# Optimization experiments

Measured on AMD Instinct MI355X. Metric: run time of the kernel, lower is better.

## Reference

```python
import jax, jax.numpy as jnp
import numpy as np

B, T, D, C, L, H = 8192, 128, 1, 1, 1, 64


def _mlp(x, w1, b1, w2, b2):
    # Linear -> Softplus -> Linear
    return jax.nn.softplus(x @ w1 + b1) @ w2 + b2


def setup_inputs() -> dict:
    key = jax.random.key(0)
    ks = jax.random.split(key, 32)
    s = 0.1

    def w(k, shape):
        return jax.random.normal(k, shape, jnp.float32) * s

    p = {}
    p["xs"] = jax.random.normal(ks[0], (T, B, D), jnp.float32)
    p["ts"] = jnp.arange(T, dtype=jnp.float32)
    p["noise_std"] = jnp.float32(5.0)
    p["eps0"] = jax.random.normal(ks[1], (B, L), jnp.float32)
    p["dW_std"] = jax.random.normal(ks[2], (T - 1, B, L), jnp.float32)
    # encoder: data -> hidden -> context
    p["ew1"] = w(ks[3], (D, H)); p["eb1"] = w(ks[4], (H,))
    p["ew2"] = w(ks[5], (H, C)); p["eb2"] = w(ks[6], (C,))
    # qz0_net: context -> 2*latent
    p["qw"] = w(ks[7], (C, 2 * L)); p["qb"] = w(ks[8], (2 * L,))
    # f_net: latent+context -> hidden -> latent
    p["fw1"] = w(ks[9], (L + C, H)); p["fb1"] = w(ks[10], (H,))
    p["fw2"] = w(ks[11], (H, L)); p["fb2"] = w(ks[12], (L,))
    # h_net: latent -> hidden -> latent
    p["hw1"] = w(ks[13], (L, H)); p["hb1"] = w(ks[14], (H,))
    p["hw2"] = w(ks[15], (H, L)); p["hb2"] = w(ks[16], (L,))
    # g_nets: L independent 1 -> hidden -> 1 -> sigmoid nets, stacked on leading L axis
    p["gw1"] = w(ks[17], (L, H)); p["gb1"] = w(ks[18], (L, H))
    p["gw2"] = w(ks[19], (L, H)); p["gb2"] = w(ks[20], (L,))
    # projector: latent -> hidden -> data
    p["pw1"] = w(ks[21], (L, H)); p["pb1"] = w(ks[22], (H,))
    p["pw2"] = w(ks[23], (H, D)); p["pb2"] = w(ks[24], (D,))
    p["pz0_mean"] = jnp.zeros((1, L), jnp.float32)
    p["pz0_logstd"] = jnp.zeros((1, L), jnp.float32)
    return p


def reference(xs, ts, noise_std, eps0, dW_std,
              ew1, eb1, ew2, eb2, qw, qb,
              fw1, fb1, fw2, fb2, hw1, hb1, hw2, hb2,
              gw1, gb1, gw2, gb2, pw1, pb1, pw2, pb2,
              pz0_mean, pz0_logstd):
    Tn = ts.shape[0]
    # ctx = flip(encoder(flip(xs)))  (encoder is pointwise in time)
    ctx = jnp.flip(_mlp(jnp.flip(xs, axis=0), ew1, eb1, ew2, eb2), axis=0)  # [T,B,C]
    qz = ctx[0] @ qw + qb
    qm, qls = jnp.split(qz, 2, axis=1)  # [B,L] each
    z0 = qm + jnp.exp(qls) * eps0

    def g_fn(z):  # per-coordinate diagonal diffusion nets
        hid = jax.nn.softplus(z[:, :, None] * gw1[None] + gb1[None])  # [B,L,H]
        return jax.nn.sigmoid(jnp.einsum('blh,lh->bl', hid, gw2) + gb2)

    def step(z, inp):
        k, dwk = inp
        t = ts[k]
        dt = ts[k + 1] - ts[k]
        idx = jnp.minimum(jnp.searchsorted(ts, t, side='right'), Tn - 1)
        c = jnp.take(ctx, idx, axis=0)  # [B,C]
        fv = _mlp(jnp.concatenate([z, c], axis=1), fw1, fb1, fw2, fb2)
        hv = _mlp(z, hw1, hb1, hw2, hb2)
        gv = g_fn(z)
        u = (fv - hv) / gv
        lr = 0.5 * jnp.sum(u * u, axis=1) * dt  # logqp path increment [B]
        z_next = z + fv * dt + gv * dwk * jnp.sqrt(dt)  # Euler-Maruyama
        return z_next, (z_next, lr)

    _, (ztail, log_ratio) = jax.lax.scan(step, z0, (jnp.arange(Tn - 1), dW_std))
    zs = jnp.concatenate([z0[None], ztail], axis=0)  # [T,B,L]
    _xs = _mlp(zs, pw1, pb1, pw2, pb2)  # [T,B,D]
    lp = -0.5 * ((xs - _xs) / noise_std) ** 2 - jnp.log(noise_std) - 0.5 * jnp.log(2 * jnp.pi)
    log_pxs = lp.sum(axis=(0, 2)).mean()
    kl = (pz0_logstd - qls) + (jnp.exp(2 * qls) + (qm - pz0_mean) ** 2) / (2 * jnp.exp(2 * pz0_logstd)) - 0.5
    logqp0 = kl.sum(axis=1).mean()
    logqp_path = log_ratio.sum(axis=0).mean()
    return (log_pxs, logqp0 + logqp_path)
```

## Files before the change

kernel.cpp:

```cpp
#include <hip/hip_runtime.h>
#include <math.h>


#define B_SZ 8192
#define T_SZ 128
#define NBLK 256

#define NT1 1025
#define NT2 1025
#define NEE 1024
#define NENT (NT1 + NT2 + NEE)

#define ENT_F 10
#define ZT_FLOATS (ENT_F * (NT1 + NT2))
#define T2_BASEF (ENT_F * NT1)
#define ET2G_OFF ZT_FLOATS
#define TABG_FLOATS (ZT_FLOATS + 2048)

#define NXI 1024
#define XSF 64.0f
#define XOF 512.0f

#if __has_builtin(__builtin_amdgcn_rcpf)
#define RCPF(x) __builtin_amdgcn_rcpf(x)
#else
#define RCPF(x) (1.0f / (x))
#endif
#if __has_builtin(__builtin_amdgcn_sqrtf)
#define SQRTF(x) __builtin_amdgcn_sqrtf(x)
#else
#define SQRTF(x) sqrtf(x)
#endif

__device__ __forceinline__ float sp_precise(float a) {
  return fmaxf(a, 0.0f) + log1pf(expf(-fabsf(a)));
}
__device__ __forceinline__ float wsum64(float v) {
  #pragma unroll
  for (int m = 1; m <= 32; m <<= 1) v += __shfl_xor(v, m);
  return v;
}
__device__ __forceinline__ float swz4(float v) {
  return __int_as_float(__builtin_amdgcn_ds_swizzle(__float_as_int(v), 0x101F));
}
template <int CTRL>
__device__ __forceinline__ float dpp_mov(float v) {
  return __int_as_float(
      __builtin_amdgcn_update_dpp(0, __float_as_int(v), CTRL, 0xF, 0xF, true));
}

__global__ __launch_bounds__(256) void build_tabs(
    const float* __restrict__ ew1, const float* __restrict__ eb1,
    const float* __restrict__ ew2, const float* __restrict__ eb2,
    const float* __restrict__ fw1, const float* __restrict__ fb1,
    const float* __restrict__ fw2, const float* __restrict__ fb2,
    const float* __restrict__ hw1, const float* __restrict__ hb1,
    const float* __restrict__ hw2, const float* __restrict__ hb2,
    const float* __restrict__ gw1, const float* __restrict__ gb1,
    const float* __restrict__ gw2, const float* __restrict__ gb2,
    const float* __restrict__ pw1, const float* __restrict__ pb1,
    const float* __restrict__ pw2, const float* __restrict__ pb2,
    float* __restrict__ tabs, int* __restrict__ ctr)
{
  const int gtid = blockIdx.x * 256 + threadIdx.x;
  if (gtid == 0) *ctr = 0;
  const int ent  = gtid >> 6;
  const int lane = threadIdx.x & 63;
  if (ent >= NENT) return;

  if (ent < NT1 + NT2) {
    const bool t1 = ent < NT1;
    const int  i  = t1 ? ent : (ent - NT1);
    const float z = t1 ? (-128.0f + (float)i * 0.25f)
                       : (-8192.0f + (float)i * 16.0f);
    const int basef = (t1 ? 0 : T2_BASEF) + ENT_F * i;

    const float az = fmaf(z, fw1[lane], fb1[lane]);
    const float wc = fw1[64 + lane], w2 = fw2[lane];
    float s0 = sp_precise(fmaf(-3.0f, wc, az)) * w2;
    float s1 = sp_precise(fmaf(-1.0f, wc, az)) * w2;
    float s2 = sp_precise(fmaf( 1.0f, wc, az)) * w2;
    float s3 = sp_precise(fmaf( 3.0f, wc, az)) * w2;
    float sh = sp_precise(fmaf(z, hw1[lane], hb1[lane])) * hw2[lane];
    float sg = sp_precise(fmaf(z, gw1[lane], gb1[lane])) * gw2[lane];
    float sp = sp_precise(fmaf(z, pw1[lane], pb1[lane])) * pw2[lane];
    s0 = wsum64(s0); s1 = wsum64(s1); s2 = wsum64(s2); s3 = wsum64(s3);
    sh = wsum64(sh); sg = wsum64(sg); sp = wsum64(sp);
    if (lane == 0) {
      const float fb = fb2[0];
      tabs[basef + 0] = s0 + fb;
      tabs[basef + 1] = s1 + fb;
      tabs[basef + 2] = s2 + fb;
      tabs[basef + 3] = s3 + fb;
      tabs[basef + 4] = sh + hb2[0];
      tabs[basef + 5] = 1.0f / (1.0f + expf(-(sg + gb2[0])));
      tabs[basef + 6] = sp + pb2[0];
      tabs[basef + 7] = 0.0f;
      tabs[basef + 8] = 0.0f;
      tabs[basef + 9] = 0.0f;
    }
  } else {
    const int i = ent - (NT1 + NT2);
    const float x0 = -8.0f + (float)i * (1.0f / 64.0f);
    const float x1 = x0 + (1.0f / 64.0f);
    const float w = ew1[lane], bb = eb1[lane], w2 = ew2[lane];
    float s0 = sp_precise(fmaf(x0, w, bb)) * w2;
    float s1 = sp_precise(fmaf(x1, w, bb)) * w2;
    s0 = wsum64(s0); s1 = wsum64(s1);
    if (lane == 0) {
      const float eb = eb2[0];
      ((float2*)(tabs + ET2G_OFF))[i] = make_float2(s0 + eb, s1 + eb);
    }
  }
}

__global__ __launch_bounds__(256) void ctx_pre(
    const float* __restrict__ xs, const float* __restrict__ tabs,
    float* __restrict__ ctx)
{
  const int i = blockIdx.x * 256 + threadIdx.x;
  const float2* et2 = (const float2*)(tabs + ET2G_OFF);
  const float s = fmaf(xs[i], XSF, XOF);
  const float sc = fminf(fmaxf(s, 0.0f), (float)(NXI - 1));
  const int ii = (int)sc;
  const float fr = s - (float)ii;
  const float2 e = et2[ii];
  ctx[i] = fmaf(fr, e.y - e.x, e.x);
}

__global__ __launch_bounds__(256) void sde_scan(
    const float* __restrict__ xs, const float* __restrict__ ts,
    const float* __restrict__ noise_std, const float* __restrict__ eps0,
    const float* __restrict__ dW, const float* __restrict__ ctx,
    const float* __restrict__ qw,  const float* __restrict__ qb,
    const float* __restrict__ fw1, const float* __restrict__ fb1,
    const float* __restrict__ fw2, const float* __restrict__ fb2,
    const float* __restrict__ hw1, const float* __restrict__ hb1,
    const float* __restrict__ hw2, const float* __restrict__ hb2,
    const float* __restrict__ gw1, const float* __restrict__ gb1,
    const float* __restrict__ gw2, const float* __restrict__ gb2,
    const float* __restrict__ pw1, const float* __restrict__ pb1,
    const float* __restrict__ pw2, const float* __restrict__ pb2,
    const float* __restrict__ pz0_mean, const float* __restrict__ pz0_logstd,
    const float* __restrict__ tabsrc,
    int* __restrict__ ctr, float* __restrict__ partA, float* __restrict__ partB,
    float* __restrict__ out)
{
  __shared__ __align__(16) float tab[ZT_FLOATS];
  __shared__ float la[256], lb[256];
  __shared__ int lastflag;

  const int tid = threadIdx.x;
  const int li  = tid & 7;
  const int b   = blockIdx.x * 32 + (tid >> 3);

  {
    const float4* s4 = (const float4*)tabsrc;
    float4* d4 = (float4*)tab;
    for (int i = tid; i < ZT_FLOATS / 4; i += 256) d4[i] = s4[i];
  }
  __syncthreads();

  const float fb2s = fb2[0], hb2s = hb2[0], gb2s = gb2[0], pb2s = pb2[0];
  const float qw0 = qw[0], qw1 = qw[1], qb0 = qb[0], qb1 = qb[1];
  const float ns = noise_std[0];
  const float inv_ns = 1.0f / ns;
  const float nh_i2 = -0.5f * inv_ns * inv_ns;
  const float pm = pz0_mean[0], pls = pz0_logstd[0];

  auto hgp_exact = [&](float z_, float& hv_, float& gv_, float& pv_) {
    float sh = 0.f, sg = 0.f, sp = 0.f;
    for (int j = 0; j < 64; ++j) {
      sh = fmaf(sp_precise(fmaf(z_, hw1[j], hb1[j])), hw2[j], sh);
      sg = fmaf(sp_precise(fmaf(z_, gw1[j], gb1[j])), gw2[j], sg);
      sp = fmaf(sp_precise(fmaf(z_, pw1[j], pb1[j])), pw2[j], sp);
    }
    hv_ = sh + hb2s;
    gv_ = 1.0f / (1.0f + expf(-(sg + gb2s)));
    pv_ = sp + pb2s;
  };
  auto f_exact = [&](float z_, float c_) {
    float s = 0.f;
    for (int j = 0; j < 64; ++j)
      s = fmaf(sp_precise(fmaf(z_, fw1[j], fmaf(c_, fw1[64 + j], fb1[j]))), fw2[j], s);
    return s + fb2s;
  };
  auto zidx = [&](float z_, int& basef_, float& frac_, bool& inr_) {
    const float s1 = fmaf(z_, 4.0f, 512.0f);
    const float s2v = fmaf(z_, 0.0625f, 512.0f);
    const bool t1 = (s1 >= 0.0f) && (s1 <= 1024.0f);
    const bool t2 = (s2v >= 0.0f) && (s2v <= 1024.0f);
    inr_ = t1 || t2;
    const float sf = t1 ? s1 : fminf(fmaxf(s2v, 0.0f), 1024.0f);
    const int fi = min((int)sf, 1023);
    basef_ = (t1 ? 0 : T2_BASEF) + ENT_F * fi;
    frac_ = sf - (float)fi;
  };

  const float c0v = ctx[b];
  const float qm  = fmaf(c0v, qw0, qb0);
  const float qls = fmaf(c0v, qw1, qb1);
  float z = fmaf(__expf(qls), eps0[b], qm);
  const float dqm = qm - pm;
  const float kl = (pls - qls)
                 + (__expf(2.0f * qls) + dqm * dqm) * (0.5f * __expf(-2.0f * pls))
                 - 0.5f;

  float xbuf0 = xs[0 * B_SZ + b], cbuf0 = ctx[0 * B_SZ + b], wbuf0 = dW[0 * B_SZ + b];
  float xbuf1 = xs[1 * B_SZ + b], cbuf1 = ctx[1 * B_SZ + b], wbuf1 = dW[1 * B_SZ + b];
  float xbuf2 = xs[2 * B_SZ + b], cbuf2 = ctx[2 * B_SZ + b], wbuf2 = dW[2 * B_SZ + b];
  float xbuf3 = xs[3 * B_SZ + b], cbuf3 = ctx[3 * B_SZ + b], wbuf3 = dW[3 * B_SZ + b];

  bool zin; int zb; float zfr;
  zidx(z, zb, zfr, zin);

  float lrs = 0.0f, lps = 0.0f;
  const int part = li & 3;
  const int loff = ((li >> 2) * ENT_F) + 2 * part;

#define STEP(K, J) { \
    const int kc = min((K) + 1, T_SZ - 1); \
    const float dt = ts[kc] - ts[(K)]; \
    const float sq = SQRTF(dt); \
    const float cc = cbuf##J; \
    const float c2 = cc * cc; \
    const float p1c = c2 - 1.0f, p3c = c2 - 9.0f; \
    const float L0 = p1c * (cc - 3.0f) * (-1.0f / 48.0f); \
    const float L1 = p3c * (cc - 1.0f) * ( 1.0f / 16.0f); \
    const float L2 = p3c * (cc + 1.0f) * (-1.0f / 16.0f); \
    const float L3 = p1c * (cc + 3.0f) * ( 1.0f / 48.0f); \
    const bool cin = fabsf(cc) <= 3.0f; \
    const float2 va = *(const float2*)(tab + zb + loff); \
    const float wz = (li < 4) ? (1.0f - zfr) : zfr; \
    const float Asel = (part == 0) ? L0 : ((part == 1) ? L2 : 1.0f); \
    const float Bsel = (part == 0) ? L1 : ((part == 1) ? L3 : 0.0f); \
    const float r0 = wz * fmaf(Asel, va.x, Bsel * va.y); \
    const float r1 = wz * va.y; \
    const float u0 = r0 + swz4(r0); \
    const float u1 = r1 + swz4(r1); \
    const float fv01 = u0 + dpp_mov<0xB1>(u0); \
    const float X = (part < 2) ? fv01 : u0; \
    const float xX = dpp_mov<0x4E>(X); \
    const float xY = dpp_mov<0x4E>(u1); \
    float FV = (part < 2) ? fv01 : xX; \
    float HV = (part == 0) ? xX : u0; \
    float GV = (part == 0) ? xY : u1; \
    float PV = (part == 1) ? xX : u0; \
    if (!(zin && cin)) FV = f_exact(z, cc); \
    if (!zin) { float he, ge, pe; hgp_exact(z, he, ge, pe); HV = he; GV = ge; PV = pe; } \
    const float gvs = fmaxf(GV, 1e-6f); \
    const float uu = (FV - HV) * RCPF(gvs); \
    lrs = fmaf((0.5f * dt) * uu, uu, lrs); \
    const float zn = fmaf(gvs * wbuf##J, sq, fmaf(FV, dt, z)); \
    const float znb = dpp_mov<0xB1>(zn); \
    z = (li & 1) ? znb : zn; \
    const float d_ = xbuf##J - PV; \
    lps = fmaf(nh_i2 * d_, d_, lps); \
     \
    const int kk_ = (K) + 4; \
    const int ixc_ = min(kk_, T_SZ - 1) * B_SZ + b; \
    const float xb_n = xs[ixc_]; \
    const float cb_n = ctx[ixc_]; \
    const float wb_n = (kk_ < T_SZ - 1) ? dW[kk_ * B_SZ + b] : 0.0f; \
    zidx(z, zb, zfr, zin); \
    xbuf##J = xb_n; cbuf##J = cb_n; wbuf##J = wb_n; \
  }

  for (int k = 0; k < T_SZ; k += 4) {
    STEP(k, 0); STEP(k + 1, 1); STEP(k + 2, 2); STEP(k + 3, 3);
  }
#undef STEP

  la[tid] = (li == 1) ? lps : 0.0f;
  lb[tid] = (li == 0) ? (kl + lrs) : 0.0f;
  __syncthreads();
  for (int s = 128; s > 0; s >>= 1) {
    if (tid < s) { la[tid] += la[tid + s]; lb[tid] += lb[tid + s]; }
    __syncthreads();
  }
  if (tid == 0) {
    partA[blockIdx.x] = la[0]; partB[blockIdx.x] = lb[0];
    __threadfence();
    lastflag = (atomicAdd(ctr, 1) == NBLK - 1) ? 1 : 0;
  }
  __syncthreads();
  if (lastflag) {
    __threadfence();
    la[tid] = partA[tid]; lb[tid] = partB[tid];
    __syncthreads();
    for (int s = 128; s > 0; s >>= 1) {
      if (tid < s) { la[tid] += la[tid + s]; lb[tid] += lb[tid + s]; }
      __syncthreads();
    }
    if (tid == 0) {
      out[0] = la[0] / (float)B_SZ
             + (float)T_SZ * (-__logf(ns) - 0.9189385332046727f);
      out[1] = lb[0] / (float)B_SZ;
    }
  }
}

extern "C" void kernel_launch(void* const* d_in, const int* in_sizes, int n_in,
                              void* d_out, int out_size, void* d_ws, size_t ws_size,
                              hipStream_t stream) {
  const float* xs        = (const float*)d_in[0];
  const float* ts        = (const float*)d_in[1];
  const float* noise_std = (const float*)d_in[2];
  const float* eps0      = (const float*)d_in[3];
  const float* dW        = (const float*)d_in[4];
  const float* ew1 = (const float*)d_in[5];
  const float* eb1 = (const float*)d_in[6];
  const float* ew2 = (const float*)d_in[7];
  const float* eb2 = (const float*)d_in[8];
  const float* qw  = (const float*)d_in[9];
  const float* qb  = (const float*)d_in[10];
  const float* fw1 = (const float*)d_in[11];
  const float* fb1 = (const float*)d_in[12];
  const float* fw2 = (const float*)d_in[13];
  const float* fb2 = (const float*)d_in[14];
  const float* hw1 = (const float*)d_in[15];
  const float* hb1 = (const float*)d_in[16];
  const float* hw2 = (const float*)d_in[17];
  const float* hb2 = (const float*)d_in[18];
  const float* gw1 = (const float*)d_in[19];
  const float* gb1 = (const float*)d_in[20];
  const float* gw2 = (const float*)d_in[21];
  const float* gb2 = (const float*)d_in[22];
  const float* pw1 = (const float*)d_in[23];
  const float* pb1 = (const float*)d_in[24];
  const float* pw2 = (const float*)d_in[25];
  const float* pb2 = (const float*)d_in[26];
  const float* pz0_mean   = (const float*)d_in[27];
  const float* pz0_logstd = (const float*)d_in[28];
  float* out = (float*)d_out;

  float* tabs  = (float*)d_ws;
  int*   ctr   = (int*)(tabs + TABG_FLOATS);
  float* partA = tabs + TABG_FLOATS + 4;
  float* partB = partA + NBLK;
  float* ctxb  = partB + NBLK;

  build_tabs<<<(NENT * 64 + 255) / 256, 256, 0, stream>>>(
      ew1, eb1, ew2, eb2, fw1, fb1, fw2, fb2,
      hw1, hb1, hw2, hb2, gw1, gb1, gw2, gb2,
      pw1, pb1, pw2, pb2, tabs, ctr);

  ctx_pre<<<(T_SZ * B_SZ) / 256, 256, 0, stream>>>(xs, tabs, ctxb);

  sde_scan<<<NBLK, 256, 0, stream>>>(
      xs, ts, noise_std, eps0, dW, ctxb, qw, qb,
      fw1, fb1, fw2, fb2, hw1, hb1, hw2, hb2,
      gw1, gb1, gw2, gb2, pw1, pb1, pw2, pb2,
      pz0_mean, pz0_logstd, tabs, ctr, partA, partB, out);
}
```

Baseline: 66.46 us.

## Use four lanes per batch element with compact 8-float table entries

Each batch element's per-step table interpolation now uses four lanes instead of eight. The table entry shrinks from 10 to 8 floats, so each lane does one float4 LDS read, and the old swizzle-plus-multiple-DPP reduction becomes one pair-swap add and one adjacent-lane move. The grid halves to 128 blocks of 64 elements, and the final cross-block reduction is guarded for the smaller partial count. This shortens the serial per-step dependency chain and cuts LDS use, but launches half as many waves, which may leave many CUs idle.

New measurement: 60.13 us. 1.11x faster.

```diff
diff --git a/kernel.cpp b/kernel.cpp
--- a/kernel.cpp
+++ b/kernel.cpp
@@ -4,14 +4,14 @@
 
 #define B_SZ 8192
 #define T_SZ 128
-#define NBLK 256
+#define NBLK 128
 
 #define NT1 1025
 #define NT2 1025
 #define NEE 1024
 #define NENT (NT1 + NT2 + NEE)
 
-#define ENT_F 10
+#define ENT_F 8
 #define ZT_FLOATS (ENT_F * (NT1 + NT2))
 #define T2_BASEF (ENT_F * NT1)
 #define ET2G_OFF ZT_FLOATS
@@ -39,9 +39,6 @@
   #pragma unroll
   for (int m = 1; m <= 32; m <<= 1) v += __shfl_xor(v, m);
   return v;
-}
-__device__ __forceinline__ float swz4(float v) {
-  return __int_as_float(__builtin_amdgcn_ds_swizzle(__float_as_int(v), 0x101F));
 }
 template <int CTRL>
 __device__ __forceinline__ float dpp_mov(float v) {
@@ -96,8 +93,6 @@
       tabs[basef + 5] = 1.0f / (1.0f + expf(-(sg + gb2[0])));
       tabs[basef + 6] = sp + pb2[0];
       tabs[basef + 7] = 0.0f;
-      tabs[basef + 8] = 0.0f;
-      tabs[basef + 9] = 0.0f;
     }
   } else {
     const int i = ent - (NT1 + NT2);
@@ -150,9 +145,9 @@
   __shared__ float la[256], lb[256];
   __shared__ int lastflag;
 
-  const int tid = threadIdx.x;
-  const int li  = tid & 7;
-  const int b   = blockIdx.x * 32 + (tid >> 3);
+  const int tid  = threadIdx.x;
+  const int part = tid & 3;
+  const int b    = blockIdx.x * 64 + (tid >> 2);
 
   {
     const float4* s4 = (const float4*)tabsrc;
@@ -215,8 +210,7 @@
   zidx(z, zb, zfr, zin);
 
   float lrs = 0.0f, lps = 0.0f;
-  const int part = li & 3;
-  const int loff = ((li >> 2) * ENT_F) + 2 * part;
+  const int loff = 4 * part;
 
 #define STEP(K, J) { \
     const int kc = min((K) + 1, T_SZ - 1); \
@@ -230,32 +224,30 @@
     const float L2 = p3c * (cc + 1.0f) * (-1.0f / 16.0f); \
     const float L3 = p1c * (cc + 3.0f) * ( 1.0f / 48.0f); \
     const bool cin = fabsf(cc) <= 3.0f; \
-    const float2 va = *(const float2*)(tab + zb + loff); \
-    const float wz = (li < 4) ? (1.0f - zfr) : zfr; \
-    const float Asel = (part == 0) ? L0 : ((part == 1) ? L2 : 1.0f); \
-    const float Bsel = (part == 0) ? L1 : ((part == 1) ? L3 : 0.0f); \
-    const float r0 = wz * fmaf(Asel, va.x, Bsel * va.y); \
-    const float r1 = wz * va.y; \
-    const float u0 = r0 + swz4(r0); \
-    const float u1 = r1 + swz4(r1); \
-    const float fv01 = u0 + dpp_mov<0xB1>(u0); \
-    const float X = (part < 2) ? fv01 : u0; \
-    const float xX = dpp_mov<0x4E>(X); \
-    const float xY = dpp_mov<0x4E>(u1); \
-    float FV = (part < 2) ? fv01 : xX; \
-    float HV = (part == 0) ? xX : u0; \
-    float GV = (part == 0) ? xY : u1; \
-    float PV = (part == 1) ? xX : u0; \
+    const float4 va = *(const float4*)(tab + zb + loff); \
+    const float wz = (part < 2) ? (1.0f - zfr) : zfr; \
+    const float dotL = fmaf(L3, va.w, fmaf(L2, va.z, fmaf(L1, va.y, L0 * va.x))); \
+    float sF = wz * dotL;           \
+    float sG = wz * va.y;           \
+    float sH = wz * va.x;           \
+    float sP = wz * va.z;           \
+    sF += dpp_mov<0x4E>(sF);        \
+    sG += dpp_mov<0x4E>(sG); \
+    sH += dpp_mov<0x4E>(sH); \
+    sP += dpp_mov<0x4E>(sP); \
+    float FV = sF;                  \
+    float GV = dpp_mov<0xB1>(sG);   \
+    float HV = dpp_mov<0xB1>(sH); \
+    float PV = sP;                  \
     if (!(zin && cin)) FV = f_exact(z, cc); \
     if (!zin) { float he, ge, pe; hgp_exact(z, he, ge, pe); HV = he; GV = ge; PV = pe; } \
     const float gvs = fmaxf(GV, 1e-6f); \
     const float uu = (FV - HV) * RCPF(gvs); \
-    lrs = fmaf((0.5f * dt) * uu, uu, lrs); \
+    lrs = fmaf((0.5f * dt) * uu, uu, lrs);         \
+    const float d_ = xbuf##J - PV; \
+    lps = fmaf(nh_i2 * d_, d_, lps);               \
     const float zn = fmaf(gvs * wbuf##J, sq, fmaf(FV, dt, z)); \
-    const float znb = dpp_mov<0xB1>(zn); \
-    z = (li & 1) ? znb : zn; \
-    const float d_ = xbuf##J - PV; \
-    lps = fmaf(nh_i2 * d_, d_, lps); \
+    z = dpp_mov<0x00>(zn);          \
      \
     const int kk_ = (K) + 4; \
     const int ixc_ = min(kk_, T_SZ - 1) * B_SZ + b; \
@@ -271,8 +263,8 @@
   }
 #undef STEP
 
-  la[tid] = (li == 1) ? lps : 0.0f;
-  lb[tid] = (li == 0) ? (kl + lrs) : 0.0f;
+  la[tid] = (part == 1) ? lps : 0.0f;
+  lb[tid] = (part == 0) ? (kl + lrs) : 0.0f;
   __syncthreads();
   for (int s = 128; s > 0; s >>= 1) {
     if (tid < s) { la[tid] += la[tid + s]; lb[tid] += lb[tid + s]; }
@@ -286,7 +278,8 @@
   __syncthreads();
   if (lastflag) {
     __threadfence();
-    la[tid] = partA[tid]; lb[tid] = partB[tid];
+    la[tid] = (tid < NBLK) ? partA[tid] : 0.0f;
+    lb[tid] = (tid < NBLK) ? partB[tid] : 0.0f;
     __syncthreads();
     for (int s = 128; s > 0; s >>= 1) {
       if (tid < s) { la[tid] += la[tid + s]; lb[tid] += lb[tid + s]; }
```
